# Kernel optimization log

Hardware: AMD Instinct MI355X
Metric: run time of the kernel (lower is better)

Reference implementation:

```python
import jax, jax.numpy as jnp
import numpy as np

ACTION_FEAT_DIM = 64
ACTION_EMB = 192
FUSION = 768
HID = 384
N_HEADS = 4
B, A = 2048, 64

gelu = lambda x: jax.nn.gelu(x, approximate=False)


def setup_inputs() -> dict:
    key = jax.random.key(0)
    ks = jax.random.split(key, 12)
    s = lambda fan_in: 1.0 / np.sqrt(fan_in)
    in_dim = ACTION_EMB + FUSION
    return {
        "action_feats": jax.random.normal(ks[0], (B, A, ACTION_FEAT_DIM), jnp.float32),
        "action_mask": jax.random.bernoulli(ks[1], 0.5, (B, A)),
        "fused": jax.random.normal(ks[2], (B, FUSION), jnp.float32),
        "phase_oh": jax.random.normal(ks[3], (B, 5), jnp.float32),
        # action encoder: Linear(64->192), GELU, Linear(192->192), GELU
        "We1": jax.random.uniform(ks[4], (ACTION_FEAT_DIM, ACTION_EMB), jnp.float32, -s(ACTION_FEAT_DIM), s(ACTION_FEAT_DIM)),
        "be1": jnp.zeros((ACTION_EMB,), jnp.float32),
        "We2": jax.random.uniform(ks[5], (ACTION_EMB, ACTION_EMB), jnp.float32, -s(ACTION_EMB), s(ACTION_EMB)),
        "be2": jnp.zeros((ACTION_EMB,), jnp.float32),
        # 4 phase heads: Linear(960->384), GELU, Linear(384->1), stacked on leading head axis
        "W1": jax.random.uniform(ks[6], (N_HEADS, in_dim, HID), jnp.float32, -s(in_dim), s(in_dim)),
        "b1": jnp.zeros((N_HEADS, HID), jnp.float32),
        "W2": jax.random.uniform(ks[7], (N_HEADS, HID), jnp.float32, -s(HID), s(HID)),
        "b2": jnp.zeros((N_HEADS,), jnp.float32),
    }


def reference(action_feats, action_mask, fused, phase_oh, We1, be1, We2, be2, W1, b1, W2, b2):
    bsz, act_count, _ = action_feats.shape
    # action encoder
    emb = gelu(gelu(action_feats @ We1 + be1) @ We2 + be2)          # [B,A,192]
    fused_rep = jnp.broadcast_to(fused[:, None, :], (bsz, act_count, fused.shape[-1]))
    inp = jnp.concatenate([emb, fused_rep], axis=-1)                 # [B,A,960]
    # dense compute of all 4 heads (faithful to original)
    h = gelu(jnp.einsum('bai,kio->bkao', inp, W1) + b1[None, :, None, :])  # [B,4,A,384]
    per_head = jnp.einsum('bkao,ko->bka', h, W2) + b2[None, :, None]       # [B,4,A]
    # phase routing: argmax over one-hot, phases >=3 map to head 3
    phase_idx = jnp.argmax(phase_oh, axis=-1)
    head_idx = jnp.where(phase_idx <= 2, phase_idx, 3)               # [B]
    logits = jnp.take_along_axis(per_head, head_idx[:, None, None], axis=1)[:, 0, :]  # [B,A]
    return jnp.where(action_mask, jnp.float32(-10000.0), logits)
```

## Files before the change

kernel.cpp:

```cpp
#include <hip/hip_runtime.h>


typedef __bf16 bf16x8 __attribute__((ext_vector_type(8)));
typedef unsigned short ushortx8 __attribute__((ext_vector_type(8)));
typedef float floatx4 __attribute__((ext_vector_type(4)));
typedef unsigned short u16;
typedef unsigned int u32;

#define B_SZ 2048
#define EMB 192
#define FUS 768
#define HID 384
#define INDIM 960
#define LDS_W 200

#define WS_FLAGS 0
#define WS_CNT 64
#define WS_HEAD 256
#define WS_LIST 8448
#define WS_WE1F 41216
#define WS_WE2F 65792
#define WS_W1F 139520
#define WS_FBF 3088640
#define WS_GSEL 6234368

__device__ __forceinline__ float bf2f(u16 u) {
  return __uint_as_float(((u32)u) << 16);
}
__device__ __forceinline__ u16 f2bf(float f) {
  u32 x = __float_as_uint(f);
  x += 0x7FFFu + ((x >> 16) & 1u);
  return (u16)(x >> 16);
}
__device__ __forceinline__ float ldf(const void* p, size_t i, int bf) {
  return bf ? bf2f(((const u16*)p)[i]) : ((const float*)p)[i];
}
__device__ __forceinline__ bf16x8 ld8(const void* p, size_t idx, int bf) {
  if (bf) return *reinterpret_cast<const bf16x8*>((const u16*)p + idx);
  const float4* f = (const float4*)((const float*)p + idx);
  float4 v0 = f[0], v1 = f[1];
  ushortx8 u;
  u[0] = f2bf(v0.x); u[1] = f2bf(v0.y); u[2] = f2bf(v0.z); u[3] = f2bf(v0.w);
  u[4] = f2bf(v1.x); u[5] = f2bf(v1.y); u[6] = f2bf(v1.z); u[7] = f2bf(v1.w);
  return __builtin_bit_cast(bf16x8, u);
}

__device__ __forceinline__ float gelu_f(float x) {
  float s = __builtin_amdgcn_fmed3f(__builtin_fmaf(0.42553f, x, 0.5f), 0.0f, 1.0f);
  return x * s;
}

__device__ __forceinline__ bool read_mask(const void* m, long long i, int fmt) {
  if (fmt == 0) return ((const int*)m)[i] != 0;
  if (fmt == 1) return ((const unsigned char*)m)[i] != 0;
  if (fmt == 2) return ((const u16*)m)[i] != 0;
  return ((const u32*)m)[i] != 0;
}

__device__ __forceinline__ int probe_bf(const void* act, int tid, int* s_bf) {
  if (tid < 64) {
    u32 w = ((const u32*)act)[tid];
    u32 h = w & 0xFFFFu;
    u32 e = (h >> 7) & 0xFFu;
    int pl = (h == 0u) || (e >= 90u && e <= 150u);
    unsigned long long nz = __ballot(h != 0u);
    unsigned long long pm = __ballot(pl);
    if (tid == 0) *s_bf = (nz != 0ULL && __popcll(pm) > 48) ? 1 : 0;
  }
  __syncthreads();
  return *s_bf;
}

#define NB_FBF 256
#define NB_WF 744
__global__ void k_prep(const void* __restrict__ act, const void* __restrict__ phase,
                       const void* __restrict__ mask, const void* __restrict__ fused,
                       const void* __restrict__ we1, const void* __restrict__ we2,
                       const void* __restrict__ w1,
                       int* __restrict__ head_idx, int* __restrict__ flags,
                       int* __restrict__ cnt, int* __restrict__ list,
                       u16* __restrict__ we1f, u16* __restrict__ we2f,
                       u16* __restrict__ w1f, u16* __restrict__ fbf) {
  __shared__ int s_bf;
  const int tid = threadIdx.x;
  const int bx = blockIdx.x;
  const int bf = probe_bf(act, tid, &s_bf);

  if (bx == 0) {
    __shared__ int sc[4][256];
    __shared__ int sfl[3];
    if (tid == 0) { sfl[0] = 0; sfl[1] = 0; sfl[2] = 0; }
    int hh[8];
    int myc[4] = {0, 0, 0, 0};
#pragma unroll
    for (int j = 0; j < 8; ++j) {
      int b = tid * 8 + j;
      float best = ldf(phase, (size_t)b * 5, bf);
      int bi = 0;
#pragma unroll
      for (int i = 1; i < 5; ++i) {
        float v = ldf(phase, (size_t)b * 5 + i, bf);
        if (v > best) { best = v; bi = i; }
      }
      int h = (bi <= 2) ? bi : 3;
      hh[j] = h;
      head_idx[b] = h;
      myc[h]++;
    }
#pragma unroll
    for (int h = 0; h < 4; ++h) sc[h][tid] = myc[h];
    __syncthreads();
    for (int off = 1; off < 256; off <<= 1) {
      int v[4];
#pragma unroll
      for (int h = 0; h < 4; ++h) v[h] = (tid >= off) ? sc[h][tid - off] : 0;
      __syncthreads();
#pragma unroll
      for (int h = 0; h < 4; ++h) sc[h][tid] += v[h];
      __syncthreads();
    }
    int start[4];
#pragma unroll
    for (int h = 0; h < 4; ++h) start[h] = sc[h][tid] - myc[h];
#pragma unroll
    for (int j = 0; j < 8; ++j) {
      int h = hh[j];
      list[h * 2048 + start[h]++] = tid * 8 + j;
    }
    if (tid == 0) {
      flags[3] = bf;
#pragma unroll
      for (int h = 0; h < 4; ++h) cnt[h] = sc[h][255];
    }
    const u32* mw = (const u32*)mask;
    u32 vi = 0, vu = 0, en = 0;
#pragma unroll
    for (int j = 0; j < 128; ++j) {
      u32 w = mw[j * 256 + tid];
      vi |= (u32)(w > 1u);
      vu |= (u32)((w & 0xFEFEFEFEu) != 0u);
      en |= (u32)((w & 0x0000FFFFu) != 0u);
    }
    if (vi) atomicOr(&sfl[0], 1);
    if (vu) atomicOr(&sfl[1], 1);
    if (en) atomicOr(&sfl[2], 1);
    __syncthreads();
    if (tid == 0) { flags[0] = sfl[0]; flags[1] = sfl[1]; flags[2] = sfl[2]; }
    return;
  }

  if (bx < 1 + NB_FBF) {
    int gid = (bx - 1) * 256 + tid;
    if (bf) {
      const uint2* s = (const uint2*)fused;
      uint2* d = (uint2*)fbf;
      for (int i = gid; i < 393216; i += NB_FBF * 256) d[i] = s[i];
    } else {
      const float4* s = (const float4*)fused;
      uint2* d = (uint2*)fbf;
      for (int i = gid; i < 393216; i += NB_FBF * 256) {
        float4 v = s[i];
        uint2 o;
        o.x = (u32)f2bf(v.x) | ((u32)f2bf(v.y) << 16);
        o.y = (u32)f2bf(v.z) | ((u32)f2bf(v.w) << 16);
        d[i] = o;
      }
    }
    return;
  }

  int fid = (bx - 1 - NB_FBF) * 256 + tid;
  int lane = fid & 63, rest = fid >> 6;
  int q = lane >> 4, nl = lane & 15;
  const void* src;
  u16* dst;
  int kk, col, ncols, dloc;
  size_t soff = 0;
  if (rest < 24) {
    src = we1; dst = we1f; dloc = fid;
    kk = rest & 1; col = (rest >> 1) * 16 + nl; ncols = EMB;
  } else if (rest < 96) {
    int r2 = rest - 24;
    src = we2; dst = we2f; dloc = (r2 << 6) | lane;
    kk = r2 % 6; col = (r2 / 6) * 16 + nl; ncols = EMB;
  } else {
    int r3 = rest - 96;
    src = w1; dst = w1f; dloc = (r3 << 6) | lane;
    kk = r3 % 30; int hn = r3 / 30;
    soff = (size_t)(hn / 24) * INDIM * HID;
    col = (hn % 24) * 16 + nl; ncols = HID;
  }
  int k0 = kk * 32 + q * 8;
  ushortx8 u;
#pragma unroll
  for (int j = 0; j < 8; ++j)
    u[j] = f2bf(ldf(src, soff + (size_t)(k0 + j) * ncols + col, bf));
  *reinterpret_cast<ushortx8*>(dst + (size_t)dloc * 8) = u;
}

__global__ __launch_bounds__(256, 4) void k_gall_sel(
    const u16* __restrict__ fbf, const u16* __restrict__ w1f,
    const void* __restrict__ b1, u16* __restrict__ gsel,
    const int* __restrict__ cnt, const int* __restrict__ list,
    const int* __restrict__ flags) {
  const int bf = flags[3];
  int c0 = cnt[0], c1 = cnt[1], c2 = cnt[2], c3 = cnt[3];
  int t0 = (c0 + 15) >> 4, t1 = (c1 + 15) >> 4, t2 = (c2 + 15) >> 4, t3 = (c3 + 15) >> 4;
  int x = blockIdx.x, h, tl;
  if (x < t0) { h = 0; tl = x; }
  else if (x < t0 + t1) { h = 1; tl = x - t0; }
  else if (x < t0 + t1 + t2) { h = 2; tl = x - t0 - t1; }
  else if (x < t0 + t1 + t2 + t3) { h = 3; tl = x - t0 - t1 - t2; }
  else return;
  int ch = (h == 0) ? c0 : (h == 1) ? c1 : (h == 2) ? c2 : c3;
  const int tid = threadIdx.x;
  const int w = tid >> 6, lane = tid & 63;
  const int nl = lane & 15, q = lane >> 4;

  int r = tl * 16 + nl;
  if (r >= ch) r = ch - 1;
  int bi = list[h * 2048 + r];
  const u16* arow = fbf + (size_t)bi * FUS;
  const int ntile = blockIdx.y * 4 + w;

  const floatx4 z4 = {0.f, 0.f, 0.f, 0.f};
  floatx4 acc = z4;
#pragma unroll 4
  for (int kk = 0; kk < 24; ++kk) {
    bf16x8 a = *reinterpret_cast<const bf16x8*>(arow + kk * 32 + q * 8);
    size_t fo = ((((size_t)h * 24 + ntile) * 30 + 6 + kk) * 64 + lane) * 8;
    bf16x8 bb = *reinterpret_cast<const bf16x8*>(w1f + fo);
    acc = __builtin_amdgcn_mfma_f32_16x16x32_bf16(a, bb, acc, 0, 0, 0);
  }
  int bi2[4];
#pragma unroll
  for (int rr = 0; rr < 4; ++rr) {
    int rm = tl * 16 + q * 4 + rr;
    if (rm >= ch) rm = ch - 1;
    bi2[rr] = list[h * 2048 + rm];
  }
  int col = ntile * 16 + nl;
  float bias = ldf(b1, (size_t)h * HID + col, bf);
#pragma unroll
  for (int rr = 0; rr < 4; ++rr)
    gsel[(size_t)bi2[rr] * HID + col] = f2bf(acc[rr] + bias);
}

__global__ __launch_bounds__(256, 4) void k_main(
    const void* __restrict__ act, const void* __restrict__ mask,
    const void* __restrict__ be1, const void* __restrict__ be2,
    const void* __restrict__ W2, const void* __restrict__ b2,
    const u16* __restrict__ we1f, const u16* __restrict__ we2f,
    const u16* __restrict__ w1f, const u16* __restrict__ gsel,
    const int* __restrict__ head_idx, const int* __restrict__ flags,
    void* __restrict__ out) {
  __shared__ __align__(16) u16 S[64 * LDS_W];
  __shared__ float red[256];
  const int b = blockIdx.x;
  const int tid = threadIdx.x;
  const int w = tid >> 6, lane = tid & 63;
  const int nl = lane & 15, q = lane >> 4;
  const int khead = head_idx[b];
  const int bf = flags[3];
  const floatx4 z4 = {0.f, 0.f, 0.f, 0.f};

  {
    floatx4 acc1[4][3];
#pragma unroll
    for (int mt = 0; mt < 4; ++mt)
#pragma unroll
      for (int nt = 0; nt < 3; ++nt) acc1[mt][nt] = z4;
#pragma unroll
    for (int kk = 0; kk < 2; ++kk) {
      bf16x8 a[4];
#pragma unroll
      for (int mt = 0; mt < 4; ++mt)
        a[mt] = ld8(act, ((size_t)b * 64 + mt * 16 + nl) * 64 + kk * 32 + q * 8, bf);
#pragma unroll
      for (int nt = 0; nt < 3; ++nt) {
        bf16x8 bfr = *reinterpret_cast<const bf16x8*>(
            we1f + (((w * 3 + nt) * 2 + kk) * 64 + lane) * 8);
#pragma unroll
        for (int mt = 0; mt < 4; ++mt)
          acc1[mt][nt] = __builtin_amdgcn_mfma_f32_16x16x32_bf16(a[mt], bfr, acc1[mt][nt], 0, 0, 0);
      }
    }
#pragma unroll
    for (int nt = 0; nt < 3; ++nt) {
      int col = w * 48 + nt * 16 + nl;
      float bias = ldf(be1, col, bf);
#pragma unroll
      for (int mt = 0; mt < 4; ++mt)
#pragma unroll
        for (int r = 0; r < 4; ++r)
          S[(mt * 16 + q * 4 + r) * LDS_W + col] = f2bf(gelu_f(acc1[mt][nt][r] + bias));
    }
  }
  __syncthreads();

  {
    floatx4 acc2[4][3];
#pragma unroll
    for (int mt = 0; mt < 4; ++mt)
#pragma unroll
      for (int nt = 0; nt < 3; ++nt) acc2[mt][nt] = z4;
#pragma unroll
    for (int kk = 0; kk < 6; ++kk) {
      bf16x8 a[4];
#pragma unroll
      for (int mt = 0; mt < 4; ++mt)
        a[mt] = *reinterpret_cast<const bf16x8*>(&S[(mt * 16 + nl) * LDS_W + kk * 32 + q * 8]);
#pragma unroll
      for (int nt = 0; nt < 3; ++nt) {
        bf16x8 bfr = *reinterpret_cast<const bf16x8*>(
            we2f + (((w * 3 + nt) * 6 + kk) * 64 + lane) * 8);
#pragma unroll
        for (int mt = 0; mt < 4; ++mt)
          acc2[mt][nt] = __builtin_amdgcn_mfma_f32_16x16x32_bf16(a[mt], bfr, acc2[mt][nt], 0, 0, 0);
      }
    }
    __syncthreads();
#pragma unroll
    for (int nt = 0; nt < 3; ++nt) {
      int col = w * 48 + nt * 16 + nl;
      float bias = ldf(be2, col, bf);
#pragma unroll
      for (int mt = 0; mt < 4; ++mt)
#pragma unroll
        for (int r = 0; r < 4; ++r)
          S[(mt * 16 + q * 4 + r) * LDS_W + col] = f2bf(gelu_f(acc2[mt][nt][r] + bias));
    }
  }
  __syncthreads();

  float partial[4][4];
#pragma unroll
  for (int mt = 0; mt < 4; ++mt)
#pragma unroll
    for (int r = 0; r < 4; ++r) partial[mt][r] = 0.f;
  const u16* grow = gsel + (size_t)b * HID;
#pragma unroll
  for (int half = 0; half < 2; ++half) {
    floatx4 acc3[4][3];
#pragma unroll
    for (int mt = 0; mt < 4; ++mt)
#pragma unroll
      for (int nt = 0; nt < 3; ++nt) acc3[mt][nt] = z4;
#pragma unroll
    for (int kk = 0; kk < 6; ++kk) {
      bf16x8 a[4];
#pragma unroll
      for (int mt = 0; mt < 4; ++mt)
        a[mt] = *reinterpret_cast<const bf16x8*>(&S[(mt * 16 + nl) * LDS_W + kk * 32 + q * 8]);
#pragma unroll
      for (int nt = 0; nt < 3; ++nt) {
        size_t fo = ((((size_t)khead * 24 + w * 6 + half * 3 + nt) * 30 + kk) * 64 + lane) * 8;
        bf16x8 bfr = *reinterpret_cast<const bf16x8*>(w1f + fo);
#pragma unroll
        for (int mt = 0; mt < 4; ++mt)
          acc3[mt][nt] = __builtin_amdgcn_mfma_f32_16x16x32_bf16(a[mt], bfr, acc3[mt][nt], 0, 0, 0);
      }
    }
#pragma unroll
    for (int nt = 0; nt < 3; ++nt) {
      int col = w * 96 + half * 48 + nt * 16 + nl;
      float g = bf2f(grow[col]);
      float w2c = ldf(W2, (size_t)khead * HID + col, bf);
#pragma unroll
      for (int mt = 0; mt < 4; ++mt)
#pragma unroll
        for (int r = 0; r < 4; ++r)
          partial[mt][r] += gelu_f(acc3[mt][nt][r] + g) * w2c;
    }
  }
#pragma unroll
  for (int off = 1; off < 16; off <<= 1)
#pragma unroll
    for (int mt = 0; mt < 4; ++mt)
#pragma unroll
      for (int r = 0; r < 4; ++r)
        partial[mt][r] += __shfl_xor(partial[mt][r], off, 16);
  if (nl == 0) {
#pragma unroll
    for (int mt = 0; mt < 4; ++mt)
#pragma unroll
      for (int r = 0; r < 4; ++r)
        red[w * 64 + mt * 16 + q * 4 + r] = partial[mt][r];
  }
  __syncthreads();

  if (tid < 64) {
    float s = red[tid] + red[64 + tid] + red[128 + tid] + red[192 + tid];
    int f0 = flags[0], f1 = flags[1], f2v = flags[2];
    int fmt = (f0 == 0) ? 0 : ((f1 == 0) ? 1 : ((f2v != 0) ? 2 : 3));
    float bb2 = ldf(b2, khead, bf);
    long long mi = (long long)b * 64 + tid;
    float v = read_mask(mask, mi, fmt) ? -10000.0f : (s + bb2);
    if (bf) ((u16*)out)[mi] = f2bf(v);
    else    ((float*)out)[mi] = v;
  }
}

extern "C" void kernel_launch(void* const* d_in, const int* in_sizes, int n_in,
                              void* d_out, int out_size, void* d_ws, size_t ws_size,
                              hipStream_t stream) {
  const void* act   = d_in[0];
  const void* mask  = d_in[1];
  const void* fused = d_in[2];
  const void* phase = d_in[3];
  const void* We1 = d_in[4];
  const void* be1 = d_in[5];
  const void* We2 = d_in[6];
  const void* be2 = d_in[7];
  const void* W1  = d_in[8];
  const void* b1  = d_in[9];
  const void* W2  = d_in[10];
  const void* b2  = d_in[11];
  char* ws = (char*)d_ws;
  int* flags    = (int*)(ws + WS_FLAGS);
  int* cnt      = (int*)(ws + WS_CNT);
  int* head_idx = (int*)(ws + WS_HEAD);
  int* list     = (int*)(ws + WS_LIST);
  u16* we1f = (u16*)(ws + WS_WE1F);
  u16* we2f = (u16*)(ws + WS_WE2F);
  u16* w1f  = (u16*)(ws + WS_W1F);
  u16* fbf  = (u16*)(ws + WS_FBF);
  u16* gsel = (u16*)(ws + WS_GSEL);

  k_prep<<<1 + NB_FBF + NB_WF, 256, 0, stream>>>(
      act, phase, mask, fused, We1, We2, W1,
      head_idx, flags, cnt, list, we1f, we2f, w1f, fbf);
  k_gall_sel<<<dim3(132, 6), 256, 0, stream>>>(fbf, w1f, b1, gsel, cnt, list, flags);
  k_main<<<B_SZ, 256, 0, stream>>>(act, mask, be1, be2, W2, b2, we1f, we2f,
                                   w1f, gsel, head_idx, flags, d_out);
}
```

Measured before the change: 191.4 us.

## Group main-kernel blocks by head and transpose weight prep through LDS

The main kernel now takes its batch row from the per-head sorted list, so consecutive blocks share the same head's W1 fragment. A strided mapping spreads each head's blocks across XCDs. This is meant to improve L2 reuse of W1 weights. The weight-fragment prep kernel now stages 32x64 tiles in shared memory for coalesced global reads, instead of strided per-thread column reads. The cost is an extra indirection and LDS round-trip, and the block count of the prep kernel must match the new tiling.

```diff
diff --git a/kernel.cpp b/kernel.cpp
--- a/kernel.cpp
+++ b/kernel.cpp
@@ -169,32 +169,33 @@
     return;
   }
 
-  int fid = (bx - 1 - NB_FBF) * 256 + tid;
-  int lane = fid & 63, rest = fid >> 6;
-  int q = lane >> 4, nl = lane & 15;
+  __shared__ u16 tile[32][68];
+  int z = bx - 1 - NB_FBF;
   const void* src;
   u16* dst;
-  int kk, col, ncols, dloc;
+  int kk, ct, ncols, kknum;
   size_t soff = 0;
-  if (rest < 24) {
-    src = we1; dst = we1f; dloc = fid;
-    kk = rest & 1; col = (rest >> 1) * 16 + nl; ncols = EMB;
-  } else if (rest < 96) {
-    int r2 = rest - 24;
-    src = we2; dst = we2f; dloc = (r2 << 6) | lane;
-    kk = r2 % 6; col = (r2 / 6) * 16 + nl; ncols = EMB;
-  } else {
-    int r3 = rest - 96;
-    src = w1; dst = w1f; dloc = (r3 << 6) | lane;
-    kk = r3 % 30; int hn = r3 / 30;
-    soff = (size_t)(hn / 24) * INDIM * HID;
-    col = (hn % 24) * 16 + nl; ncols = HID;
-  }
-  int k0 = kk * 32 + q * 8;
+  int hn = 0;
+  if (z < 6)       { src = we1; dst = we1f; kk = z / 3; ct = z % 3; ncols = EMB; kknum = 2; }
+  else if (z < 24) { int z2 = z - 6;  src = we2; dst = we2f; kk = z2 / 3; ct = z2 % 3; ncols = EMB; kknum = 6; }
+  else             { int z3 = z - 24; int h = z3 / 180, rem = z3 % 180;
+                     src = w1; dst = w1f; kk = rem / 6; ct = rem % 6; ncols = HID; kknum = 30;
+                     soff = (size_t)h * INDIM * HID; hn = h * 24; }
+  const int k0 = kk * 32, c0 = ct * 64;
+#pragma unroll
+  for (int j = 0; j < 8; ++j) {
+    int idx = j * 256 + tid;
+    int r = idx >> 6, c = idx & 63;
+    tile[r][c] = f2bf(ldf(src, soff + (size_t)(k0 + r) * ncols + c0 + c, bf));
+  }
+  __syncthreads();
+  int lane = tid & 63, ntl = tid >> 6;
+  int nl = lane & 15, q = lane >> 4;
   ushortx8 u;
 #pragma unroll
-  for (int j = 0; j < 8; ++j)
-    u[j] = f2bf(ldf(src, soff + (size_t)(k0 + j) * ncols + col, bf));
+  for (int j = 0; j < 8; ++j) u[j] = tile[q * 8 + j][ntl * 16 + nl];
+  int ntile = ct * 4 + ntl;
+  int dloc = ((hn + ntile) * kknum + kk) * 64 + lane;
   *reinterpret_cast<ushortx8*>(dst + (size_t)dloc * 8) = u;
 }
 
@@ -252,17 +253,24 @@
     const void* __restrict__ W2, const void* __restrict__ b2,
     const u16* __restrict__ we1f, const u16* __restrict__ we2f,
     const u16* __restrict__ w1f, const u16* __restrict__ gsel,
-    const int* __restrict__ head_idx, const int* __restrict__ flags,
-    void* __restrict__ out) {
+    const int* __restrict__ cnt, const int* __restrict__ list,
+    const int* __restrict__ flags, void* __restrict__ out) {
   __shared__ __align__(16) u16 S[64 * LDS_W];
   __shared__ float red[256];
-  const int b = blockIdx.x;
   const int tid = threadIdx.x;
   const int w = tid >> 6, lane = tid & 63;
   const int nl = lane & 15, q = lane >> 4;
-  const int khead = head_idx[b];
   const int bf = flags[3];
   const floatx4 z4 = {0.f, 0.f, 0.f, 0.f};
+
+  const int g = blockIdx.x;
+  const int idx = (g & 7) * 256 + (g >> 3);
+  const int p1 = cnt[0], p2 = p1 + cnt[1], p3 = p2 + cnt[2];
+  int khead, b;
+  if (idx < p1)      { khead = 0; b = list[idx]; }
+  else if (idx < p2) { khead = 1; b = list[2048 + idx - p1]; }
+  else if (idx < p3) { khead = 2; b = list[4096 + idx - p2]; }
+  else               { khead = 3; b = list[6144 + idx - p3]; }
 
   {
     floatx4 acc1[4][3];
@@ -364,13 +372,13 @@
 #pragma unroll
     for (int nt = 0; nt < 3; ++nt) {
       int col = w * 96 + half * 48 + nt * 16 + nl;
-      float g = bf2f(grow[col]);
+      float g2 = bf2f(grow[col]);
       float w2c = ldf(W2, (size_t)khead * HID + col, bf);
 #pragma unroll
       for (int mt = 0; mt < 4; ++mt)
 #pragma unroll
         for (int r = 0; r < 4; ++r)
-          partial[mt][r] += gelu_f(acc3[mt][nt][r] + g) * w2c;
+          partial[mt][r] += gelu_f(acc3[mt][nt][r] + g2) * w2c;
     }
   }
 #pragma unroll
@@ -432,5 +440,5 @@
       head_idx, flags, cnt, list, we1f, we2f, w1f, fbf);
   k_gall_sel<<<dim3(132, 6), 256, 0, stream>>>(fbf, w1f, b1, gsel, cnt, list, flags);
   k_main<<<B_SZ, 256, 0, stream>>>(act, mask, be1, be2, W2, b2, we1f, we2f,
-                                   w1f, gsel, head_idx, flags, d_out);
-}
+                                   w1f, gsel, cnt, list, flags, d_out);
+}
```

Result: no change. 191.9 us (+0.3%).
